# Kernel tuning notes

Measured on AMD Instinct MI355X. Metric: run time of the kernel, lower is better.

## Reference

```python
import jax, jax.numpy as jnp
from jax import lax
import numpy as np

HEADS, SAMPLES = 4, 8
B, C, D, H, W = 1, 64, 16, 64, 64
HD = C // HEADS  # head_dim = 16
BN_EPS = 1e-5


def conv3d(x, w, b=None, pad=0):
    out = lax.conv_general_dilated(
        x, w, (1, 1, 1), [(pad, pad)] * 3,
        dimension_numbers=("NCDHW", "OIDHW", "NCDHW"))
    if b is not None:
        out = out + b[None, :, None, None, None]
    return out


def trilinear_sample(vol, grid):
    # vol: [Dv,Hv,Wv,Cc]; grid: [...,3] with torch grid_sample semantics:
    # grid[...,0] -> x (W axis), grid[...,1] -> y (H axis), grid[...,2] -> z (D axis)
    # align_corners=True, padding_mode='border'. Returns [..., Cc].
    Dv, Hv, Wv, _ = vol.shape
    ix = (grid[..., 0] + 1.0) * 0.5 * (Wv - 1)
    iy = (grid[..., 1] + 1.0) * 0.5 * (Hv - 1)
    iz = (grid[..., 2] + 1.0) * 0.5 * (Dv - 1)
    x0 = jnp.floor(ix); y0 = jnp.floor(iy); z0 = jnp.floor(iz)
    wx = (ix - x0)[..., None]; wy = (iy - y0)[..., None]; wz = (iz - z0)[..., None]
    x0i = jnp.clip(x0.astype(jnp.int32), 0, Wv - 1); x1i = jnp.clip(x0i + 1, 0, Wv - 1)
    y0i = jnp.clip(y0.astype(jnp.int32), 0, Hv - 1); y1i = jnp.clip(y0i + 1, 0, Hv - 1)
    z0i = jnp.clip(z0.astype(jnp.int32), 0, Dv - 1); z1i = jnp.clip(z0i + 1, 0, Dv - 1)
    g = lambda z, y, x: vol[z, y, x]
    out = (g(z0i, y0i, x0i) * (1 - wz) * (1 - wy) * (1 - wx)
           + g(z0i, y0i, x1i) * (1 - wz) * (1 - wy) * wx
           + g(z0i, y1i, x0i) * (1 - wz) * wy * (1 - wx)
           + g(z0i, y1i, x1i) * (1 - wz) * wy * wx
           + g(z1i, y0i, x0i) * wz * (1 - wy) * (1 - wx)
           + g(z1i, y0i, x1i) * wz * (1 - wy) * wx
           + g(z1i, y1i, x0i) * wz * wy * (1 - wx)
           + g(z1i, y1i, x1i) * wz * wy * wx)
    return out


def t_deform(feat_prev, feat_curr, p):
    b, c, d, h, w = feat_curr.shape
    kv = conv3d(feat_prev, p["kv_w"], p["kv_b"])          # [B,2C,D,H,W]
    q = conv3d(feat_curr, p["q_w"], p["q_b"])              # [B,C,D,H,W]
    # offset branch: conv3x3 -> GELU(exact) -> conv3x3(no bias) -> tanh
    o = conv3d(feat_curr, p["off1_w"], p["off1_b"], pad=1)
    o = jax.nn.gelu(o, approximate=False)
    o = jnp.tanh(conv3d(o, p["off2_w"], None, pad=1))      # [B,M*S*3,D,H,W]
    off = o.reshape(b, HEADS, SAMPLES, 3, d, h, w).transpose(0, 1, 4, 5, 6, 2, 3)  # [B,M,D,H,W,S,3]
    zz, yy, xx = jnp.meshgrid(jnp.linspace(-1, 1, d), jnp.linspace(-1, 1, h),
                              jnp.linspace(-1, 1, w), indexing="ij")
    base = jnp.stack((zz, yy, xx), axis=-1).astype(feat_curr.dtype)  # [D,H,W,3]
    scale = jnp.array([d, h, w], dtype=feat_curr.dtype)
    grid = base[None, None, :, :, :, None, :] + off / scale
    grid = jnp.clip(grid, -1.0, 1.0)
    grid = grid.transpose(0, 1, 5, 2, 3, 4, 6).reshape(b * HEADS, SAMPLES, d, h, w, 3)
    # channels-last per (batch,head) volume; avoids torch's explicit repeat over samples
    vols = kv.reshape(b, HEADS, 2 * HD, d, h, w).transpose(0, 1, 3, 4, 5, 2)
    vols = vols.reshape(b * HEADS, d, h, w, 2 * HD)
    sampled = jax.vmap(trilinear_sample)(vols, grid)        # [B*M,S,D,H,W,2*HD]
    sampled = sampled.reshape(b, HEADS, SAMPLES, d, h, w, 2 * HD)
    key, value = sampled[..., :HD], sampled[..., HD:]
    qh = q.reshape(b, HEADS, HD, d, h, w) * (HD ** -0.5)
    attn = jnp.einsum("bmcdhw,bmsdhwc->bmsdhw", qh, key)
    attn = jax.nn.softmax(attn, axis=2)
    fused = jnp.einsum("bmsdhw,bmsdhwc->bmcdhw", attn, value).reshape(b, c, d, h, w)
    out = conv3d(fused, p["out_w"], p["out_b"])
    # BatchNorm3d (eval: running stats) + ReLU
    inv = lax.rsqrt(p["bn_var"] + BN_EPS)
    out = (out - p["bn_mean"][None, :, None, None, None]) * (inv * p["bn_gamma"])[None, :, None, None, None] \
          + p["bn_beta"][None, :, None, None, None]
    return jax.nn.relu(out)


def setup_inputs() -> dict:
    key = jax.random.key(0)
    ks = jax.random.split(key, 16)
    r = lambda k, shp, s=0.05: (jax.random.normal(k, shp, dtype=jnp.float32) * s)
    return {
        "mid_feat": jax.random.normal(ks[0], (B, C, D, H, W), dtype=jnp.float32),
        "occ_feat": jax.random.normal(ks[1], (B, C, D, H, W), dtype=jnp.float32),
        "prev_feat": jax.random.normal(ks[2], (B, C, D, H, W), dtype=jnp.float32),
        "off1_w": r(ks[3], (C, C, 3, 3, 3)), "off1_b": r(ks[4], (C,)),
        "off2_w": r(ks[5], (HEADS * SAMPLES * 3, C, 3, 3, 3)),
        "kv_w": r(ks[6], (2 * C, C, 1, 1, 1)), "kv_b": r(ks[7], (2 * C,)),
        "q_w": r(ks[8], (C, C, 1, 1, 1)), "q_b": r(ks[9], (C,)),
        "out_w": r(ks[10], (C, C, 1, 1, 1)), "out_b": r(ks[11], (C,)),
        "bn_gamma": jnp.ones((C,), jnp.float32), "bn_beta": jnp.zeros((C,), jnp.float32),
        "bn_mean": jnp.zeros((C,), jnp.float32), "bn_var": jnp.ones((C,), jnp.float32),
    }


def reference(mid_feat, occ_feat, prev_feat, off1_w, off1_b, off2_w, kv_w, kv_b,
              q_w, q_b, out_w, out_b, bn_gamma, bn_beta, bn_mean, bn_var):
    p = dict(off1_w=off1_w, off1_b=off1_b, off2_w=off2_w, kv_w=kv_w, kv_b=kv_b,
             q_w=q_w, q_b=q_b, out_w=out_w, out_b=out_b, bn_gamma=bn_gamma,
             bn_beta=bn_beta, bn_mean=bn_mean, bn_var=bn_var)
    d1 = t_deform(mid_feat, occ_feat, p)
    d2 = t_deform(mid_feat, prev_feat, p)
    return jnp.concatenate([mid_feat, d1, d2], axis=1)  # [B,3C,D,H,W]
```

## Files before the change

### kernel.cpp

```cpp
#include <hip/hip_runtime.h>
#include <math.h>

#define DD 16
#define HH 64
#define WW 64
#define VV (DD*HH*WW)
#define CC 64
#define NHEADS 4
#define NSAMP 8
#define HDIM 16

typedef unsigned int uint;
typedef unsigned short ushort;
typedef __attribute__((ext_vector_type(8))) short bf16x8;
typedef __attribute__((ext_vector_type(4))) float f32x4;

__device__ __forceinline__ float clampf(float v, float lo, float hi){ return fminf(fmaxf(v, lo), hi); }
__device__ __forceinline__ int imin(int a, int b){ return a < b ? a : b; }
__device__ __forceinline__ int imax(int a, int b){ return a > b ? a : b; }

__device__ __forceinline__ ushort f2bf(float f){
  uint u = __float_as_uint(f);
  uint r = (u + 0x7fffu + ((u>>16)&1u)) >> 16;
  return (ushort)r;
}
__device__ __forceinline__ uint packbf2(float a, float b){
  return (uint)f2bf(a) | ((uint)f2bf(b) << 16);
}
__device__ __forceinline__ float bflo(uint u){ return __uint_as_float(u << 16); }
__device__ __forceinline__ float bfhi(uint u){ return __uint_as_float(u & 0xffff0000u); }
__device__ __forceinline__ float bf2f(ushort u){ return __uint_as_float((uint)u << 16); }

__device__ __forceinline__ float fast_tanh(float x){
  float e = __expf(2.f*x);
  return 1.f - 2.f/(e + 1.f);
}

__global__ void repack_wmfma(const float* __restrict__ w, uint* __restrict__ o, int MG){
  int U = blockIdx.x*256 + threadIdx.x;
  int total = 54*MG*256;
  if (U >= total) return;
  int j2 = U & 3;
  int m  = (U>>2) & 15;
  int q  = (U>>6) & 3;
  int rest = U >> 8;
  int g = rest % MG;
  int s = rest / MG;
  int tap = s >> 1, h = s & 1;
  int co = g*16 + m;
  int ci = h*32 + q*8 + j2*2;
  int base = co*1728 + ci*27 + tap;
  o[U] = packbf2(w[base], w[base + 27]);
}
__global__ void repack_w1mfma(const float* __restrict__ w, uint* __restrict__ o, int MT){
  int U = blockIdx.x*256 + threadIdx.x;
  int total = 2*MT*256;
  if (U >= total) return;
  int j2 = U & 3;
  int lane = (U>>2) & 63;
  int frag = U >> 8;
  int mt = frag % MT;
  int ks = frag / MT;
  int q = lane >> 4, m = lane & 15;
  int co = mt*16 + m;
  int ci = ks*32 + q*8 + j2*2;
  o[U] = packbf2(w[co*CC + ci], w[co*CC + ci + 1]);
}

template<int CO, int EPI>
__global__ __launch_bounds__(256) void conv1_mfma(
    const float* __restrict__ xa, const float* __restrict__ xb,
    const uint* __restrict__ wA, const float* __restrict__ bias,
    void* __restrict__ outp)
{
  constexpr int MT = CO/16;
  constexpr int MW = MT/4;
  __shared__ ushort xt[64*72];
  int tid = threadIdx.x;
  int lane = tid & 63;
  int g = __builtin_amdgcn_readfirstlane(tid >> 6);
  int q = lane >> 4, n = lane & 15;
  int call = blockIdx.x >> 10;
  int v0 = (blockIdx.x & 1023) * 64;
  const float* x = call ? xb : xa;
  for (int it = tid; it < 64*32; it += 256){
    int vox = it & 63; int cp = it >> 6;
    float a = x[(size_t)(2*cp)*VV + v0 + vox];
    float b = x[(size_t)(2*cp+1)*VV + v0 + vox];
    *reinterpret_cast<uint*>(&xt[vox*72 + 2*cp]) = packbf2(a,b);
  }
  __syncthreads();
  f32x4 acc[MW][4];
  #pragma unroll
  for (int mw=0;mw<MW;mw++)
    #pragma unroll
    for (int nt=0;nt<4;nt++){ acc[mw][nt].x=0.f; acc[mw][nt].y=0.f; acc[mw][nt].z=0.f; acc[mw][nt].w=0.f; }
  const char* ldsb = reinterpret_cast<const char*>(xt);
  const char* wac  = reinterpret_cast<const char*>(wA);
  #pragma unroll
  for (int ks=0; ks<2; ks++){
    bf16x8 bfr[4];
    #pragma unroll
    for (int nt=0; nt<4; nt++)
      bfr[nt] = *reinterpret_cast<const bf16x8*>(ldsb + ((nt*16+n)*144 + q*16 + ks*64));
    #pragma unroll
    for (int mw=0; mw<MW; mw++){
      int mt = g*MW + mw;
      bf16x8 af = *reinterpret_cast<const bf16x8*>(wac + (size_t)((ks*MT + mt)*64 + lane)*16);
      #pragma unroll
      for (int nt=0; nt<4; nt++)
        acc[mw][nt] = __builtin_amdgcn_mfma_f32_16x16x32_bf16(af, bfr[nt], acc[mw][nt], 0, 0, 0);
    }
  }
  if (EPI == 0){
    #pragma unroll
    for (int mw=0; mw<MW; mw++){
      int mt = g*MW + mw;
      int cob = mt*16 + q*4;
      #pragma unroll
      for (int nt=0; nt<4; nt++){
        int v = v0 + nt*16 + n;
        float r0 = acc[mw][nt].x + bias[cob+0];
        float r1 = acc[mw][nt].y + bias[cob+1];
        float r2 = acc[mw][nt].z + bias[cob+2];
        float r3 = acc[mw][nt].w + bias[cob+3];
        int z = v >> 12, y = (v >> 6) & 63, xx = v & 63;
        int head = cob >> 5;
        uint* vols = (uint*)outp;
        uint2 pk; pk.x = packbf2(r0,r1); pk.y = packbf2(r2,r3);
        *reinterpret_cast<uint2*>(vols + ((size_t)head*VV + (size_t)(y*WW+xx)*DD + z)*16 + ((cob&31)>>1)) = pk;
      }
    }
  } else {
    __syncthreads();
    ushort* xr = xt;
    int cob = g*16 + q*4;
    #pragma unroll
    for (int nt=0; nt<4; nt++){
      int vox = nt*16 + n;
      uint2 pk;
      pk.x = packbf2((acc[0][nt].x + bias[cob+0])*0.25f, (acc[0][nt].y + bias[cob+1])*0.25f);
      pk.y = packbf2((acc[0][nt].z + bias[cob+2])*0.25f, (acc[0][nt].w + bias[cob+3])*0.25f);
      *reinterpret_cast<uint2*>(&xr[vox*64 + cob]) = pk;
    }
    __syncthreads();
    char* ob = (char*)((ushort*)outp + (size_t)call*CC*VV) + (size_t)v0*128;
    const char* lb = reinterpret_cast<const char*>(xr);
    #pragma unroll
    for (int k=0; k<2; k++){
      int idx = tid + k*256;
      *reinterpret_cast<uint4*>(ob + idx*16) = *reinterpret_cast<const uint4*>(lb + idx*16);
    }
  }
}

template<int CO, int INPK, int OUTPK>
__global__ __launch_bounds__(256) void conv3_mfma(
    const float* __restrict__ xa, const float* __restrict__ xb,
    const uint* __restrict__ xpk,
    const uint* __restrict__ wA, const float* __restrict__ bias,
    void* __restrict__ outp)
{
  constexpr int MG = CO/16;
  constexpr int MROW = CO/32;
  __shared__ ushort xh[300*40];
  int tid = threadIdx.x;
  int lane = tid & 63;
  int w = __builtin_amdgcn_readfirstlane(tid >> 6);
  int q = lane >> 4, n = lane & 15;
  int bid = blockIdx.x;
  int xcd = bid & 7, islot = bid >> 3;
  int call = islot >> 7;
  int z = xcd*2 + ((islot >> 6) & 1);
  int rem = islot & 63;
  int by = (rem >> 3) << 3, bx = (rem & 7) << 3;

  const float* xin = call ? xb : xa;
  const uint* xinp = xpk + (size_t)call*32*VV;

  int mbase = (w & 1) * MROW;
  int np = w >> 1;
  int lo[2];
  #pragma unroll
  for (int nt=0;nt<2;nt++){
    int vox = (np*2+nt)*16 + n;
    lo[nt] = ((vox>>3)*10 + (vox&7))*80 + q*16;
  }
  f32x4 acc[MROW][2];
  #pragma unroll
  for (int mr=0;mr<MROW;mr++)
    #pragma unroll
    for (int nt=0;nt<2;nt++){ acc[mr][nt].x=0.f; acc[mr][nt].y=0.f; acc[mr][nt].z=0.f; acc[mr][nt].w=0.f; }

  const char* ldsb = reinterpret_cast<const char*>(xh);
  const char* wac  = reinterpret_cast<const char*>(wA);

  #pragma unroll 1
  for (int h=0; h<2; h++){
    if (h) __syncthreads();
    for (int it = tid; it < 2400; it += 256){
      int cg = it / 300; int pos = it - cg*300;
      int dz = pos/100; int r = pos - dz*100; int dy = r/10; int dxx = r - dy*10;
      int gz = z + dz - 1, gy = by + dy - 1, gx = bx + dxx - 1;
      bool ok = (gz>=0 && gz<DD && gy>=0 && gy<HH && gx>=0 && gx<WW);
      uint2 pk; pk.x = 0u; pk.y = 0u;
      if (ok){
        size_t gv = (size_t)((gz*HH+gy)*WW + gx);
        if (INPK){
          int cp0 = h*16 + cg*2;
          pk.x = xinp[(size_t)cp0*VV + gv];
          pk.y = xinp[(size_t)(cp0+1)*VV + gv];
        } else {
          int ci0 = h*32 + cg*4;
          float v0 = xin[(size_t)(ci0  )*VV + gv];
          float v1 = xin[(size_t)(ci0+1)*VV + gv];
          float v2 = xin[(size_t)(ci0+2)*VV + gv];
          float v3 = xin[(size_t)(ci0+3)*VV + gv];
          pk.x = packbf2(v0,v1); pk.y = packbf2(v2,v3);
        }
      }
      *reinterpret_cast<uint2*>(&xh[pos*40 + cg*4]) = pk;
    }
    __syncthreads();
    #pragma unroll 3
    for (int tap=0; tap<27; tap++){
      int dz = tap/9; int r9 = tap - dz*9; int dy = r9/3; int dxx = r9 - dy*3;
      int stepOff = (dz*100 + dy*10 + dxx)*80;
      int s = tap*2 + h;
      bf16x8 af[MROW];
      #pragma unroll
      for (int mr=0;mr<MROW;mr++)
        af[mr] = *reinterpret_cast<const bf16x8*>(wac + (size_t)((s*MG + mbase+mr)*64 + lane)*16);
      bf16x8 bf[2];
      #pragma unroll
      for (int nt=0;nt<2;nt++)
        bf[nt] = *reinterpret_cast<const bf16x8*>(ldsb + (lo[nt] + stepOff));
      #pragma unroll
      for (int mr=0;mr<MROW;mr++)
        #pragma unroll
        for (int nt=0;nt<2;nt++)
          acc[mr][nt] = __builtin_amdgcn_mfma_f32_16x16x32_bf16(af[mr], bf[nt], acc[mr][nt], 0, 0, 0);
    }
  }

  if (OUTPK == 1){
    #pragma unroll
    for (int mr=0; mr<MROW; mr++){
      int cob = (mbase+mr)*16 + q*4;
      #pragma unroll
      for (int nt=0; nt<2; nt++){
        int vox = (np*2+nt)*16 + n;
        int vy = by + (vox>>3), vx = bx + (vox&7);
        size_t gv = (size_t)((z*HH + vy)*WW + vx);
        float r0 = acc[mr][nt].x + bias[cob+0];
        float r1 = acc[mr][nt].y + bias[cob+1];
        float r2 = acc[mr][nt].z + bias[cob+2];
        float r3 = acc[mr][nt].w + bias[cob+3];
        r0 = 0.5f*r0*(1.f + erff(r0*0.70710678118654752f));
        r1 = 0.5f*r1*(1.f + erff(r1*0.70710678118654752f));
        r2 = 0.5f*r2*(1.f + erff(r2*0.70710678118654752f));
        r3 = 0.5f*r3*(1.f + erff(r3*0.70710678118654752f));
        uint* dst = (uint*)outp + (size_t)call*32*VV;
        dst[(size_t)(cob>>1)*VV + gv]     = packbf2(r0,r1);
        dst[(size_t)((cob>>1)+1)*VV + gv] = packbf2(r2,r3);
      }
    }
  } else {
    __syncthreads();
    ushort* xr = xh;
    #pragma unroll
    for (int mr=0; mr<MROW; mr++){
      int cob = (mbase+mr)*16 + q*4;
      #pragma unroll
      for (int nt=0; nt<2; nt++){
        int vox = (np*2+nt)*16 + n;
        uint2 pk;
        pk.x = packbf2(fast_tanh(acc[mr][nt].x), fast_tanh(acc[mr][nt].y));
        pk.y = packbf2(fast_tanh(acc[mr][nt].z), fast_tanh(acc[mr][nt].w));
        *reinterpret_cast<uint2*>(&xr[vox*96 + cob]) = pk;
      }
    }
    __syncthreads();
    ushort* dst = (ushort*)outp + (size_t)call*96*VV;
    const char* lb = reinterpret_cast<const char*>(xr);
    #pragma unroll
    for (int k=0; k<3; k++){
      int idx = tid + k*256;
      int row = idx/96;
      int off = idx - row*96;
      size_t gb = (size_t)((z*HH + by + row)*WW + bx)*192 + (size_t)off*16;
      *reinterpret_cast<uint4*>((char*)dst + gb) = *reinterpret_cast<const uint4*>(lb + idx*16);
    }
  }
}

struct Geom { int x0,x1,y0,y1,z0,z1; float wx,wy,wz; };
__device__ __forceinline__ Geom make_geom(float zb, float yb, float xb,
                                          float o0, float o1, float o2){
  float g0 = clampf(zb + o0*(1.f/16.f), -1.f, 1.f);
  float g1 = clampf(yb + o1*(1.f/64.f), -1.f, 1.f);
  float g2 = clampf(xb + o2*(1.f/64.f), -1.f, 1.f);
  float ix = (g0+1.f)*0.5f*63.f;
  float iy = (g1+1.f)*0.5f*63.f;
  float iz = (g2+1.f)*0.5f*15.f;
  float fx=floorf(ix), fy=floorf(iy), fz=floorf(iz);
  Geom g;
  g.wx = ix-fx; g.wy = iy-fy; g.wz = iz-fz;
  g.x0 = imin(imax((int)fx,0), WW-1); g.x1 = imin(g.x0+1, WW-1);
  g.y0 = imin(imax((int)fy,0), HH-1); g.y1 = imin(g.y0+1, HH-1);
  g.z0 = imin(imax((int)fz,0), DD-1); g.z1 = imin(g.z0+1, DD-1);
  return g;
}

__global__ __launch_bounds__(256) void sample_attn_kernel(
    const ushort* __restrict__ qbuf, const ushort* __restrict__ offbuf,
    const uint* __restrict__ vols, const uint* __restrict__ woA,
    const float* __restrict__ outb, const float* __restrict__ bng,
    const float* __restrict__ bnb, const float* __restrict__ bnm,
    const float* __restrict__ bnv, float* __restrict__ dout)
{
  __shared__ ushort fsb[16*72];
  int t = threadIdx.x;
  int lane = t & 63;
  int m = __builtin_amdgcn_readfirstlane(t >> 6);
  int slot = lane >> 2;
  int r = lane & 3;
  int bid = blockIdx.x;
  int xcd = bid & 7, islot = bid >> 3;
  int call = islot >> 9;
  int z = xcd*2 + ((islot >> 8) & 1);
  int rem = islot & 255;
  int y = rem >> 2;
  int x0 = (rem & 3) << 4;
  int x = x0 + slot;
  int vbase = (z*HH + y)*WW + x0;
  int v = vbase + slot;

  const ushort* qb = qbuf   + (size_t)call*CC*VV;
  const ushort* ob = offbuf + (size_t)call*96*VV;

  uint4 qu = *reinterpret_cast<const uint4*>(qb + (size_t)v*64 + m*16 + (r&1)*8);
  float qf[8];
  qf[0]=bflo(qu.x); qf[1]=bfhi(qu.x); qf[2]=bflo(qu.y); qf[3]=bfhi(qu.y);
  qf[4]=bflo(qu.z); qf[5]=bfhi(qu.z); qf[6]=bflo(qu.w); qf[7]=bfhi(qu.w);

  uint ou[12];
  {
    const uint4* op4 = reinterpret_cast<const uint4*>(ob + (size_t)v*96 + m*24);
    uint4 a = op4[0], b4 = op4[1], c4 = op4[2];
    ou[0]=a.x;  ou[1]=a.y;  ou[2]=a.z;  ou[3]=a.w;
    ou[4]=b4.x; ou[5]=b4.y; ou[6]=b4.z; ou[7]=b4.w;
    ou[8]=c4.x; ou[9]=c4.y; ou[10]=c4.z; ou[11]=c4.w;
  }

  float zbf = -1.f + (float)z*(2.f/15.f);
  float ybf = -1.f + (float)y*(2.f/63.f);
  float xbf = -1.f + (float)x*(2.f/63.f);

  const char* volb = reinterpret_cast<const char*>(vols) + (size_t)m*VV*64;
  float roleK = (r < 2) ? 1.f : 0.f;
  float lrun = 0.f;
  float fused[8];
  #pragma unroll
  for (int c=0;c<8;c++) fused[c]=0.f;

  #pragma unroll
  for (int s=0;s<NSAMP;s++){
    int i0 = 3*s, i1 = 3*s+1, i2 = 3*s+2;
    float o0 = (i0&1) ? bfhi(ou[i0>>1]) : bflo(ou[i0>>1]);
    float o1 = (i1&1) ? bfhi(ou[i1>>1]) : bflo(ou[i1>>1]);
    float o2 = (i2&1) ? bfhi(ou[i2>>1]) : bflo(ou[i2>>1]);
    Geom g = make_geom(zbf,ybf,xbf,o0,o1,o2);
    int tz0 = g.z0*64 + r*16;
    int tz1 = g.z1*64 + r*16;
    float wx1 = g.wx, wx0 = 1.f-g.wx;
    float wy1 = g.wy, wy0 = 1.f-g.wy;
    float wz1 = g.wz, wz0 = 1.f-g.wz;
    float acc[8];
    #pragma unroll
    for (int c=0;c<8;c++) acc[c]=0.f;
    #pragma unroll
    for (int ky=0;ky<2;ky++)
    #pragma unroll
    for (int kx=0;kx<2;kx++){
      int cy = ky? g.y1:g.y0, cx = kx? g.x1:g.x0;
      float wyx = (ky? wy1:wy0)*(kx? wx1:wx0);
      float a0 = wyx*wz0, a1 = wyx*wz1;
      uint wzp;
      asm("v_cvt_pk_bf16_f32 %0, %1, %2" : "=v"(wzp) : "v"(a0), "v"(a1));
      int tb = ((cy<<6) + cx) << 10;
      const char* p = volb + tb;
      uint4 u0 = *reinterpret_cast<const uint4*>(p + tz0);
      uint4 u1 = *reinterpret_cast<const uint4*>(p + tz1);
      uint plo, phi;
      plo = __builtin_amdgcn_perm(u1.x, u0.x, 0x05040100u);
      phi = __builtin_amdgcn_perm(u1.x, u0.x, 0x07060302u);
      asm("v_dot2_f32_bf16 %0, %1, %2, %0" : "+v"(acc[0]) : "v"(plo), "v"(wzp));
      asm("v_dot2_f32_bf16 %0, %1, %2, %0" : "+v"(acc[1]) : "v"(phi), "v"(wzp));
      plo = __builtin_amdgcn_perm(u1.y, u0.y, 0x05040100u);
      phi = __builtin_amdgcn_perm(u1.y, u0.y, 0x07060302u);
      asm("v_dot2_f32_bf16 %0, %1, %2, %0" : "+v"(acc[2]) : "v"(plo), "v"(wzp));
      asm("v_dot2_f32_bf16 %0, %1, %2, %0" : "+v"(acc[3]) : "v"(phi), "v"(wzp));
      plo = __builtin_amdgcn_perm(u1.z, u0.z, 0x05040100u);
      phi = __builtin_amdgcn_perm(u1.z, u0.z, 0x07060302u);
      asm("v_dot2_f32_bf16 %0, %1, %2, %0" : "+v"(acc[4]) : "v"(plo), "v"(wzp));
      asm("v_dot2_f32_bf16 %0, %1, %2, %0" : "+v"(acc[5]) : "v"(phi), "v"(wzp));
      plo = __builtin_amdgcn_perm(u1.w, u0.w, 0x05040100u);
      phi = __builtin_amdgcn_perm(u1.w, u0.w, 0x07060302u);
      asm("v_dot2_f32_bf16 %0, %1, %2, %0" : "+v"(acc[6]) : "v"(plo), "v"(wzp));
      asm("v_dot2_f32_bf16 %0, %1, %2, %0" : "+v"(acc[7]) : "v"(phi), "v"(wzp));
    }
    float h = qf[0]*acc[0]+qf[1]*acc[1]+qf[2]*acc[2]+qf[3]*acc[3]
            + qf[4]*acc[4]+qf[5]*acc[5]+qf[6]*acc[6]+qf[7]*acc[7];
    h *= roleK;
    h += __shfl_xor(h, 1);
    h += __shfl_xor(h, 2);
    float e = __expf(h);
    lrun += e;
    #pragma unroll
    for (int c=0;c<8;c++) fused[c] += e*acc[c];
  }
  float isum = 1.f/lrun;
  if (r >= 2){
    uint4 pk;
    pk.x = packbf2(fused[0]*isum, fused[1]*isum);
    pk.y = packbf2(fused[2]*isum, fused[3]*isum);
    pk.z = packbf2(fused[4]*isum, fused[5]*isum);
    pk.w = packbf2(fused[6]*isum, fused[7]*isum);
    *reinterpret_cast<uint4*>(&fsb[slot*72 + m*16 + (r&1)*8]) = pk;
  }
  __syncthreads();

  int qq = lane >> 4, n = lane & 15;
  f32x4 acco;
  acco.x=0.f; acco.y=0.f; acco.z=0.f; acco.w=0.f;
  const char* ldsb = reinterpret_cast<const char*>(fsb);
  const char* wac  = reinterpret_cast<const char*>(woA);
  #pragma unroll
  for (int ks=0; ks<2; ks++){
    bf16x8 af = *reinterpret_cast<const bf16x8*>(wac + (size_t)((ks*4 + m)*64 + lane)*16);
    bf16x8 bfv = *reinterpret_cast<const bf16x8*>(ldsb + (n*144 + qq*16 + ks*64));
    acco = __builtin_amdgcn_mfma_f32_16x16x32_bf16(af, bfv, acco, 0, 0, 0);
  }
  int choff = 64 + call*64;
  #pragma unroll
  for (int rr=0; rr<4; rr++){
    int co = m*16 + qq*4 + rr;
    float inv = rsqrtf(bnv[co] + 1e-5f) * bng[co];
    float val = (acco[rr] + outb[co] - bnm[co]) * inv + bnb[co];
    val = fmaxf(val, 0.f);
    dout[(size_t)(choff+co)*VV + vbase + n] = val;
  }
}

extern "C" void kernel_launch(void* const* d_in, const int* in_sizes, int n_in,
                              void* d_out, int out_size, void* d_ws, size_t ws_size,
                              hipStream_t stream){
  (void)in_sizes; (void)n_in; (void)out_size; (void)ws_size;
  const float* mid  = (const float*)d_in[0];
  const float* occ  = (const float*)d_in[1];
  const float* prev = (const float*)d_in[2];
  const float* off1w= (const float*)d_in[3];
  const float* off1b= (const float*)d_in[4];
  const float* off2w= (const float*)d_in[5];
  const float* kvw  = (const float*)d_in[6];
  const float* kvb  = (const float*)d_in[7];
  const float* qw   = (const float*)d_in[8];
  const float* qb   = (const float*)d_in[9];
  const float* outw = (const float*)d_in[10];
  const float* outb = (const float*)d_in[11];
  const float* bng  = (const float*)d_in[12];
  const float* bnb  = (const float*)d_in[13];
  const float* bnm  = (const float*)d_in[14];
  const float* bnv  = (const float*)d_in[15];
  float* out = (float*)d_out;

  uint*   vols  = (uint*)d_ws;
  ushort* qbuf  = (ushort*)(vols + (size_t)4*VV*16);
  uint*   o1pk  = (uint*)(qbuf + (size_t)2*CC*VV);
  ushort* offb  = (ushort*)(o1pk + (size_t)2*32*VV);
  uint*   wA1   = (uint*)(offb + (size_t)2*96*VV);
  uint*   wA2   = wA1 + 55296;
  uint*   wo    = wA2 + 82944;
  uint*   wkv   = wo  + 2048;
  uint*   wq    = wkv + 4096;

  repack_wmfma<<<(55296+255)/256, 256, 0, stream>>>(off1w, wA1, 4);
  repack_wmfma<<<(82944+255)/256, 256, 0, stream>>>(off2w, wA2, 6);
  repack_w1mfma<<<8, 256, 0, stream>>>(outw, wo, 4);
  repack_w1mfma<<<16, 256, 0, stream>>>(kvw, wkv, 8);
  repack_w1mfma<<<8, 256, 0, stream>>>(qw, wq, 4);
  conv1_mfma<128,0><<<1024, 256, 0, stream>>>(mid, mid, wkv, kvb, (void*)vols);
  hipMemcpyAsync(out, mid, (size_t)CC*VV*sizeof(float), hipMemcpyDeviceToDevice, stream);
  conv1_mfma<64,1><<<2048, 256, 0, stream>>>(occ, prev, wq, qb, (void*)qbuf);
  conv3_mfma<64,0,1><<<2048, 256, 0, stream>>>(occ, prev, (const uint*)nullptr, wA1, off1b, (void*)o1pk);
  conv3_mfma<96,1,0><<<2048, 256, 0, stream>>>((const float*)nullptr, (const float*)nullptr, o1pk, wA2, off1b, (void*)offb);
  sample_attn_kernel<<<8192, 256, 0, stream>>>(qbuf, offb, vols, wo,
      outb, bng, bnb, bnm, bnv, out);
}
```

Measured before the change: 363.3 us.

## Prepack inputs to bf16, z-pair sample volume, and double-buffer conv3 halo loads

A new kernel packs occ/prev inputs to channel-paired bf16 once, and the q 1x1 conv and first 3x3 conv read that instead of converting fp32 per block. The KV volume is re-laid out so the z and z+1 values are interleaved, letting the sampler fetch both depths in one contiguous 32-byte read without perm instructions. conv3 now loads the second channel half into registers while computing the first, overlapping global loads with MFMA work. The sampler also drops the lower clamp on indices, and the change adds two extra passes and more workspace memory.

Result: no change. 368.7 us (+1.5%).

```diff
diff --git a/kernel.cpp b/kernel.cpp
--- a/kernel.cpp
+++ b/kernel.cpp
@@ -17,7 +17,6 @@
 
 __device__ __forceinline__ float clampf(float v, float lo, float hi){ return fminf(fmaxf(v, lo), hi); }
 __device__ __forceinline__ int imin(int a, int b){ return a < b ? a : b; }
-__device__ __forceinline__ int imax(int a, int b){ return a > b ? a : b; }
 
 __device__ __forceinline__ ushort f2bf(float f){
   uint u = __float_as_uint(f);
@@ -34,6 +33,39 @@
 __device__ __forceinline__ float fast_tanh(float x){
   float e = __expf(2.f*x);
   return 1.f - 2.f/(e + 1.f);
+}
+
+__global__ __launch_bounds__(256) void pack_in(const float* __restrict__ a,
+                                               const float* __restrict__ b,
+                                               uint* __restrict__ o){
+  int idx = blockIdx.x*256 + threadIdx.x;
+  int v4 = (idx & (VV/4 - 1)) * 4;
+  int rest = idx >> 14;
+  int cp = rest & 31;
+  int call = rest >> 5;
+  const float* x = call ? b : a;
+  float4 f0 = *reinterpret_cast<const float4*>(x + (size_t)(2*cp)*VV + v4);
+  float4 f1 = *reinterpret_cast<const float4*>(x + (size_t)(2*cp+1)*VV + v4);
+  uint4 pk;
+  pk.x = packbf2(f0.x, f1.x);
+  pk.y = packbf2(f0.y, f1.y);
+  pk.z = packbf2(f0.z, f1.z);
+  pk.w = packbf2(f0.w, f1.w);
+  *reinterpret_cast<uint4*>(o + (size_t)(call*32+cp)*VV + v4) = pk;
+}
+
+__global__ __launch_bounds__(256) void zpair(const uint* __restrict__ vin,
+                                             uint* __restrict__ vout){
+  int idx = blockIdx.x*256 + threadIdx.x;
+  int j = idx & 15;
+  int rest = idx >> 4;
+  int z = rest & 15;
+  uint uz  = vin[idx];
+  uint uz1 = vin[(z < 15) ? idx + 16 : idx];
+  uint lo = __builtin_amdgcn_perm(uz1, uz, 0x05040100u);
+  uint hi = __builtin_amdgcn_perm(uz1, uz, 0x07060302u);
+  uint2 pk; pk.x = lo; pk.y = hi;
+  *reinterpret_cast<uint2*>(vout + ((size_t)rest << 5) + 2*j) = pk;
 }
 
 __global__ void repack_wmfma(const float* __restrict__ w, uint* __restrict__ o, int MG){
@@ -69,7 +101,7 @@
 
 template<int CO, int EPI>
 __global__ __launch_bounds__(256) void conv1_mfma(
-    const float* __restrict__ xa, const float* __restrict__ xb,
+    const void* __restrict__ xa, const void* __restrict__ xb,
     const uint* __restrict__ wA, const float* __restrict__ bias,
     void* __restrict__ outp)
 {
@@ -82,12 +114,20 @@
   int q = lane >> 4, n = lane & 15;
   int call = blockIdx.x >> 10;
   int v0 = (blockIdx.x & 1023) * 64;
-  const float* x = call ? xb : xa;
-  for (int it = tid; it < 64*32; it += 256){
-    int vox = it & 63; int cp = it >> 6;
-    float a = x[(size_t)(2*cp)*VV + v0 + vox];
-    float b = x[(size_t)(2*cp+1)*VV + v0 + vox];
-    *reinterpret_cast<uint*>(&xt[vox*72 + 2*cp]) = packbf2(a,b);
+  if constexpr (EPI == 0){
+    const float* x = call ? (const float*)xb : (const float*)xa;
+    for (int it = tid; it < 64*32; it += 256){
+      int vox = it & 63; int cp = it >> 6;
+      float a = x[(size_t)(2*cp)*VV + v0 + vox];
+      float b = x[(size_t)(2*cp+1)*VV + v0 + vox];
+      *reinterpret_cast<uint*>(&xt[vox*72 + 2*cp]) = packbf2(a,b);
+    }
+  } else {
+    const uint* xp = (const uint*)xa + (size_t)call*32*VV;
+    for (int it = tid; it < 64*32; it += 256){
+      int vox = it & 63; int cp = it >> 6;
+      *reinterpret_cast<uint*>(&xt[vox*72 + 2*cp]) = xp[(size_t)cp*VV + v0 + vox];
+    }
   }
   __syncthreads();
   f32x4 acc[MW][4];
@@ -112,7 +152,7 @@
         acc[mw][nt] = __builtin_amdgcn_mfma_f32_16x16x32_bf16(af, bfr[nt], acc[mw][nt], 0, 0, 0);
     }
   }
-  if (EPI == 0){
+  if constexpr (EPI == 0){
     #pragma unroll
     for (int mw=0; mw<MW; mw++){
       int mt = g*MW + mw;
@@ -154,9 +194,8 @@
   }
 }
 
-template<int CO, int INPK, int OUTPK>
+template<int CO, int OUTPK>
 __global__ __launch_bounds__(256) void conv3_mfma(
-    const float* __restrict__ xa, const float* __restrict__ xb,
     const uint* __restrict__ xpk,
     const uint* __restrict__ wA, const float* __restrict__ bias,
     void* __restrict__ outp)
@@ -175,7 +214,6 @@
   int rem = islot & 63;
   int by = (rem >> 3) << 3, bx = (rem & 7) << 3;
 
-  const float* xin = call ? xb : xa;
   const uint* xinp = xpk + (size_t)call*32*VV;
 
   int mbase = (w & 1) * MROW;
@@ -195,33 +233,38 @@
   const char* ldsb = reinterpret_cast<const char*>(xh);
   const char* wac  = reinterpret_cast<const char*>(wA);
 
-  #pragma unroll 1
-  for (int h=0; h<2; h++){
-    if (h) __syncthreads();
-    for (int it = tid; it < 2400; it += 256){
-      int cg = it / 300; int pos = it - cg*300;
-      int dz = pos/100; int r = pos - dz*100; int dy = r/10; int dxx = r - dy*10;
-      int gz = z + dz - 1, gy = by + dy - 1, gx = bx + dxx - 1;
-      bool ok = (gz>=0 && gz<DD && gy>=0 && gy<HH && gx>=0 && gx<WW);
-      uint2 pk; pk.x = 0u; pk.y = 0u;
-      if (ok){
-        size_t gv = (size_t)((gz*HH+gy)*WW + gx);
-        if (INPK){
+  uint pa[10], pb[10]; int lofs[10];
+  auto load_half = [&](int h){
+    #pragma unroll
+    for (int k=0;k<10;k++){
+      int it = tid + k*256;
+      if (it < 2400){
+        int cg = it/300; int pos = it - cg*300;
+        int dz = pos/100; int rr = pos - dz*100; int dy = rr/10; int dxx = rr - dy*10;
+        int gz = z + dz - 1, gy = by + dy - 1, gx = bx + dxx - 1;
+        lofs[k] = pos*40 + cg*4;
+        uint a = 0u, b = 0u;
+        if (gz>=0 && gz<DD && gy>=0 && gy<HH && gx>=0 && gx<WW){
+          size_t gv = (size_t)((gz*HH+gy)*WW + gx);
           int cp0 = h*16 + cg*2;
-          pk.x = xinp[(size_t)cp0*VV + gv];
-          pk.y = xinp[(size_t)(cp0+1)*VV + gv];
-        } else {
-          int ci0 = h*32 + cg*4;
-          float v0 = xin[(size_t)(ci0  )*VV + gv];
-          float v1 = xin[(size_t)(ci0+1)*VV + gv];
-          float v2 = xin[(size_t)(ci0+2)*VV + gv];
-          float v3 = xin[(size_t)(ci0+3)*VV + gv];
-          pk.x = packbf2(v0,v1); pk.y = packbf2(v2,v3);
+          a = xinp[(size_t)cp0*VV + gv];
+          b = xinp[(size_t)(cp0+1)*VV + gv];
         }
+        pa[k] = a; pb[k] = b;
       }
-      *reinterpret_cast<uint2*>(&xh[pos*40 + cg*4]) = pk;
-    }
-    __syncthreads();
+    }
+  };
+  auto write_half = [&](){
+    #pragma unroll
+    for (int k=0;k<10;k++){
+      int it = tid + k*256;
+      if (it < 2400){
+        uint2 pk; pk.x = pa[k]; pk.y = pb[k];
+        *reinterpret_cast<uint2*>(&xh[lofs[k]]) = pk;
+      }
+    }
+  };
+  auto compute_half = [&](int h){
     #pragma unroll 3
     for (int tap=0; tap<27; tap++){
       int dz = tap/9; int r9 = tap - dz*9; int dy = r9/3; int dxx = r9 - dy*3;
@@ -241,7 +284,17 @@
         for (int nt=0;nt<2;nt++)
           acc[mr][nt] = __builtin_amdgcn_mfma_f32_16x16x32_bf16(af[mr], bf[nt], acc[mr][nt], 0, 0, 0);
     }
-  }
+  };
+
+  load_half(0);
+  write_half();
+  __syncthreads();
+  load_half(1);
+  compute_half(0);
+  __syncthreads();
+  write_half();
+  __syncthreads();
+  compute_half(1);
 
   if (OUTPK == 1){
     #pragma unroll
@@ -306,9 +359,9 @@
   float fx=floorf(ix), fy=floorf(iy), fz=floorf(iz);
   Geom g;
   g.wx = ix-fx; g.wy = iy-fy; g.wz = iz-fz;
-  g.x0 = imin(imax((int)fx,0), WW-1); g.x1 = imin(g.x0+1, WW-1);
-  g.y0 = imin(imax((int)fy,0), HH-1); g.y1 = imin(g.y0+1, HH-1);
-  g.z0 = imin(imax((int)fz,0), DD-1); g.z1 = imin(g.z0+1, DD-1);
+  g.x0 = (int)fx; g.x1 = imin(g.x0+1, WW-1);
+  g.y0 = (int)fy; g.y1 = imin(g.y0+1, HH-1);
+  g.z0 = (int)fz; g.z1 = imin(g.z0+1, DD-1);
   return g;
 }
 
@@ -357,7 +410,7 @@
   float ybf = -1.f + (float)y*(2.f/63.f);
   float xbf = -1.f + (float)x*(2.f/63.f);
 
-  const char* volb = reinterpret_cast<const char*>(vols) + (size_t)m*VV*64;
+  const char* volb = reinterpret_cast<const char*>(vols) + (size_t)m*VV*128;
   float roleK = (r < 2) ? 1.f : 0.f;
   float lrun = 0.f;
   float fused[8];
@@ -371,8 +424,7 @@
     float o1 = (i1&1) ? bfhi(ou[i1>>1]) : bflo(ou[i1>>1]);
     float o2 = (i2&1) ? bfhi(ou[i2>>1]) : bflo(ou[i2>>1]);
     Geom g = make_geom(zbf,ybf,xbf,o0,o1,o2);
-    int tz0 = g.z0*64 + r*16;
-    int tz1 = g.z1*64 + r*16;
+    const char* pz = volb + (g.z0*128 + r*32);
     float wx1 = g.wx, wx0 = 1.f-g.wx;
     float wy1 = g.wy, wy0 = 1.f-g.wy;
     float wz1 = g.wz, wz0 = 1.f-g.wz;
@@ -388,27 +440,17 @@
       float a0 = wyx*wz0, a1 = wyx*wz1;
       uint wzp;
       asm("v_cvt_pk_bf16_f32 %0, %1, %2" : "=v"(wzp) : "v"(a0), "v"(a1));
-      int tb = ((cy<<6) + cx) << 10;
-      const char* p = volb + tb;
-      uint4 u0 = *reinterpret_cast<const uint4*>(p + tz0);
-      uint4 u1 = *reinterpret_cast<const uint4*>(p + tz1);
-      uint plo, phi;
-      plo = __builtin_amdgcn_perm(u1.x, u0.x, 0x05040100u);
-      phi = __builtin_amdgcn_perm(u1.x, u0.x, 0x07060302u);
-      asm("v_dot2_f32_bf16 %0, %1, %2, %0" : "+v"(acc[0]) : "v"(plo), "v"(wzp));
-      asm("v_dot2_f32_bf16 %0, %1, %2, %0" : "+v"(acc[1]) : "v"(phi), "v"(wzp));
-      plo = __builtin_amdgcn_perm(u1.y, u0.y, 0x05040100u);
-      phi = __builtin_amdgcn_perm(u1.y, u0.y, 0x07060302u);
-      asm("v_dot2_f32_bf16 %0, %1, %2, %0" : "+v"(acc[2]) : "v"(plo), "v"(wzp));
-      asm("v_dot2_f32_bf16 %0, %1, %2, %0" : "+v"(acc[3]) : "v"(phi), "v"(wzp));
-      plo = __builtin_amdgcn_perm(u1.z, u0.z, 0x05040100u);
-      phi = __builtin_amdgcn_perm(u1.z, u0.z, 0x07060302u);
-      asm("v_dot2_f32_bf16 %0, %1, %2, %0" : "+v"(acc[4]) : "v"(plo), "v"(wzp));
-      asm("v_dot2_f32_bf16 %0, %1, %2, %0" : "+v"(acc[5]) : "v"(phi), "v"(wzp));
-      plo = __builtin_amdgcn_perm(u1.w, u0.w, 0x05040100u);
-      phi = __builtin_amdgcn_perm(u1.w, u0.w, 0x07060302u);
-      asm("v_dot2_f32_bf16 %0, %1, %2, %0" : "+v"(acc[6]) : "v"(plo), "v"(wzp));
-      asm("v_dot2_f32_bf16 %0, %1, %2, %0" : "+v"(acc[7]) : "v"(phi), "v"(wzp));
+      const char* p = pz + (((cy<<6) + cx) << 11);
+      uint4 u0 = *reinterpret_cast<const uint4*>(p);
+      uint4 u1 = *reinterpret_cast<const uint4*>(p + 16);
+      asm("v_dot2_f32_bf16 %0, %1, %2, %0" : "+v"(acc[0]) : "v"(u0.x), "v"(wzp));
+      asm("v_dot2_f32_bf16 %0, %1, %2, %0" : "+v"(acc[1]) : "v"(u0.y), "v"(wzp));
+      asm("v_dot2_f32_bf16 %0, %1, %2, %0" : "+v"(acc[2]) : "v"(u0.z), "v"(wzp));
+      asm("v_dot2_f32_bf16 %0, %1, %2, %0" : "+v"(acc[3]) : "v"(u0.w), "v"(wzp));
+      asm("v_dot2_f32_bf16 %0, %1, %2, %0" : "+v"(acc[4]) : "v"(u1.x), "v"(wzp));
+      asm("v_dot2_f32_bf16 %0, %1, %2, %0" : "+v"(acc[5]) : "v"(u1.y), "v"(wzp));
+      asm("v_dot2_f32_bf16 %0, %1, %2, %0" : "+v"(acc[6]) : "v"(u1.z), "v"(wzp));
+      asm("v_dot2_f32_bf16 %0, %1, %2, %0" : "+v"(acc[7]) : "v"(u1.w), "v"(wzp));
     }
     float h = qf[0]*acc[0]+qf[1]*acc[1]+qf[2]*acc[2]+qf[3]*acc[3]
             + qf[4]*acc[4]+qf[5]*acc[5]+qf[6]*acc[6]+qf[7]*acc[7];
@@ -484,17 +526,21 @@
   uint*   wo    = wA2 + 82944;
   uint*   wkv   = wo  + 2048;
   uint*   wq    = wkv + 4096;
-
+  uint*   o0pk  = wq  + 2048;
+  uint*   vols2 = o0pk + (size_t)2*32*VV;
+
+  pack_in<<<4096, 256, 0, stream>>>(occ, prev, o0pk);
   repack_wmfma<<<(55296+255)/256, 256, 0, stream>>>(off1w, wA1, 4);
   repack_wmfma<<<(82944+255)/256, 256, 0, stream>>>(off2w, wA2, 6);
   repack_w1mfma<<<8, 256, 0, stream>>>(outw, wo, 4);
   repack_w1mfma<<<16, 256, 0, stream>>>(kvw, wkv, 8);
   repack_w1mfma<<<8, 256, 0, stream>>>(qw, wq, 4);
   conv1_mfma<128,0><<<1024, 256, 0, stream>>>(mid, mid, wkv, kvb, (void*)vols);
+  zpair<<<16384, 256, 0, stream>>>(vols, vols2);
   hipMemcpyAsync(out, mid, (size_t)CC*VV*sizeof(float), hipMemcpyDeviceToDevice, stream);
-  conv1_mfma<64,1><<<2048, 256, 0, stream>>>(occ, prev, wq, qb, (void*)qbuf);
-  conv3_mfma<64,0,1><<<2048, 256, 0, stream>>>(occ, prev, (const uint*)nullptr, wA1, off1b, (void*)o1pk);
-  conv3_mfma<96,1,0><<<2048, 256, 0, stream>>>((const float*)nullptr, (const float*)nullptr, o1pk, wA2, off1b, (void*)offb);
-  sample_attn_kernel<<<8192, 256, 0, stream>>>(qbuf, offb, vols, wo,
+  conv1_mfma<64,1><<<2048, 256, 0, stream>>>(o0pk, nullptr, wq, qb, (void*)qbuf);
+  conv3_mfma<64,1><<<2048, 256, 0, stream>>>(o0pk, wA1, off1b, (void*)o1pk);
+  conv3_mfma<96,0><<<2048, 256, 0, stream>>>(o1pk, wA2, off1b, (void*)offb);
+  sample_attn_kernel<<<8192, 256, 0, stream>>>(qbuf, offb, vols2, wo,
       outb, bng, bnb, bnm, bnv, out);
 }
```
